# Optimization experiments

Hardware: AMD Instinct MI355X
Metric: run time of the kernel (lower is better)

The kernel has to match this reference:

```python
import jax, jax.numpy as jnp
import numpy as np

N_CHILDS = 50000
N_EDGES = 500000
NODE_FEAT = 256
NUM_SEM = 57
HID = 256
EDGE_FEAT = 64
EDGE_TYPES = 4
NUM_ITERS = 2


def setup_inputs() -> dict:
    key = jax.random.key(0)
    ks = jax.random.split(key, 12)
    d_in = NODE_FEAT + NUM_SEM            # 313
    d_ne = 2 * HID + EDGE_FEAT + EDGE_TYPES  # 580
    d_par = HID * (NUM_ITERS + 1)         # 768
    def lin(k, fan_in, fan_out):
        kw, kb = jax.random.split(k)
        s = 1.0 / np.sqrt(fan_in)
        return (jax.random.uniform(kw, (fan_in, fan_out), jnp.float32, -s, s),
                jax.random.uniform(kb, (fan_out,), jnp.float32, -s, s))
    W_child, b_child = lin(ks[0], d_in, HID)
    W_ne0, b_ne0 = lin(ks[1], d_ne, HID)
    W_ne1, b_ne1 = lin(ks[2], d_ne, HID)
    W_parent, b_parent = lin(ks[3], d_par, NODE_FEAT)
    return {
        "child_feats": jax.random.normal(ks[4], (1, N_CHILDS, d_in), jnp.float32),
        "child_exists": jnp.ones((1, N_CHILDS, 1), jnp.float32),
        "edge_type_onehot": jax.random.normal(ks[5], (1, N_EDGES, EDGE_TYPES), jnp.float32),
        "edge_feats": jax.random.normal(ks[6], (1, N_EDGES, EDGE_FEAT), jnp.float32),
        "edge_indices": jax.random.randint(ks[7], (1, N_EDGES, 2), 0, N_CHILDS, jnp.int64),
        "W_child": W_child, "b_child": b_child,
        "W_ne0": W_ne0, "b_ne0": b_ne0,
        "W_ne1": W_ne1, "b_ne1": b_ne1,
        "W_parent": W_parent, "b_parent": b_parent,
    }


def reference(child_feats, child_exists, edge_type_onehot, edge_feats, edge_indices,
              W_child, b_child, W_ne0, b_ne0, W_ne1, b_ne1, W_parent, b_parent):
    n = child_feats.shape[1]
    # node embedding: linear + relu, mask non-existent children
    x = jax.nn.relu(jnp.einsum('bnd,dh->bnh', child_feats, W_child) + b_child)
    x = x * child_exists                              # [1, N, H]
    iter_parent = [x.max(axis=1)]                     # symmetric_type == 'max'
    ef = jnp.concatenate([edge_type_onehot, edge_feats], axis=2)[0]  # [E, 4+64]
    src = edge_indices[0, :, 0]
    dst = edge_indices[0, :, 1]
    cnt = jax.ops.segment_sum(jnp.ones((src.shape[0],), x.dtype), src, num_segments=n)
    denom = jnp.maximum(cnt, 1.0)[:, None]            # scatter_mean clamp
    for W, b in ((W_ne0, b_ne0), (W_ne1, b_ne1)):
        nef = jnp.concatenate([x[0, src], x[0, dst], ef], axis=1)  # [E, 580]
        nef = jax.nn.relu(nef @ W + b)                # [E, H]
        # edge_symmetric_type == 'avg': scatter_mean over source index
        x = (jax.ops.segment_sum(nef, src, num_segments=n) / denom)[None]
        iter_parent.append(x.max(axis=1))
    parent = jnp.concatenate(iter_parent, axis=1)     # [1, H*(iters+1)]
    return jax.nn.relu(parent @ W_parent + b_parent)  # [1, node_feat_size]
```

## Files before the change

### kernel.cpp

```cpp
#include <hip/hip_runtime.h>

#define NC   50000
#define NE   500000
#define NEP  (NE + 64)
#define DIN  313
#define DNE  580
#define KPC  320
#define KB   96
#define NB_SCAN 196

typedef __attribute__((ext_vector_type(8))) short bf16x8;
typedef __attribute__((ext_vector_type(4))) float f32x4;

static __device__ __forceinline__ unsigned short f2bf(float f) {
    unsigned u = __float_as_uint(f);
    unsigned r = (u + 0x7fff + ((u >> 16) & 1)) >> 16;
    return (unsigned short)r;
}
static __device__ __forceinline__ float bf2f(unsigned short u) {
    return __uint_as_float(((unsigned)u) << 16);
}
static __device__ __forceinline__ void gload_lds16(const unsigned short* g, unsigned short* l) {
    __builtin_amdgcn_global_load_lds(
        (const __attribute__((address_space(1))) unsigned int*)(g),
        (__attribute__((address_space(3))) unsigned int*)(l), 16, 0, 0);
}

__global__ __launch_bounds__(256) void prep_w_kernel(
    const float* __restrict__ W0, const float* __restrict__ W1,
    const float* __restrict__ Wc,
    unsigned short* __restrict__ Wpt, unsigned short* __restrict__ Wbt,
    unsigned short* __restrict__ Wct)
{
    int b = blockIdx.x;
    if (b < 1024) {
        int layer = b >> 9, n2 = b & 511;
        const float* W = layer ? W1 : W0;
        unsigned short* dst = Wpt + (size_t)layer * 512 * 256 + (size_t)n2 * 256;
        int t = threadIdx.x;
        int ch = t >> 5, s = (t >> 3) & 3, j = t & 7;
        int gk = ch * 32 + ((s ^ (n2 & 3)) * 8) + j;
        float v = (n2 < 256) ? W[(size_t)gk * 256 + n2] : W[(size_t)(256 + gk) * 256 + (n2 - 256)];
        dst[t] = f2bf(v);
    } else if (b < 1536) {
        int idx = b - 1024;
        int layer = idx >> 8, n = idx & 255;
        const float* W = layer ? W1 : W0;
        unsigned short* dst = Wbt + (size_t)layer * 256 * KB + (size_t)n * KB;
        int t = threadIdx.x;
        if (t < KB) {
            int ch = t >> 5, s = (t >> 3) & 3, j = t & 7;
            int gk = ch * 32 + ((s ^ (n & 3)) * 8) + j;
            float v = (512 + gk < DNE) ? W[(size_t)(512 + gk) * 256 + n] : 0.0f;
            dst[t] = f2bf(v);
        }
    } else {
        int n = b - 1536;
        unsigned short* dst = Wct + (size_t)n * KPC;
        for (int t = threadIdx.x; t < KPC; t += 256) {
            int ch = t >> 5, s = (t >> 3) & 3, j = t & 7;
            int gk = ch * 32 + ((s ^ (n & 3)) * 8) + j;
            float v = (gk < DIN) ? Wc[(size_t)gk * 256 + n] : 0.0f;
            dst[t] = f2bf(v);
        }
    }
}

__global__ __launch_bounds__(256, 4) void child_mfma_kernel(
    const float* __restrict__ cf, const float* __restrict__ exists,
    const unsigned short* __restrict__ Wct, const float* __restrict__ bias,
    unsigned short* __restrict__ xb, float* __restrict__ pmax)
{
    __shared__ unsigned short sA[64][40];
    __shared__ unsigned short sB[256][32];
    __shared__ float smax[256];

    const int tid = threadIdx.x, lane = tid & 63, wid = tid >> 6;
    const int wm = wid >> 1, wn = wid & 1, l15 = lane & 15, l4 = lane >> 4;
    const int node0 = blockIdx.x * 64;
    const int arow = tid >> 2, s3 = tid & 3;

    smax[tid] = 0.0f;

    f32x4 acc[2][8];
    #pragma unroll
    for (int mi = 0; mi < 2; ++mi)
        #pragma unroll
        for (int ni = 0; ni < 8; ++ni)
            acc[mi][ni] = (f32x4){0.f, 0.f, 0.f, 0.f};

    int nodeA = node0 + arow; if (nodeA >= NC) nodeA = NC - 1;

    for (int ch = 0; ch < 10; ++ch) {
        #pragma unroll
        for (int i = 0; i < 4; ++i) {
            int n = (wid << 6) + (i << 4) + (lane >> 2);
            gload_lds16(Wct + (size_t)n * KPC + ch * 32 + (lane & 3) * 8,
                        &sB[(wid << 6) + (i << 4)][0]);
        }
        {
            int gk0 = ch * 32 + s3 * 8;
            union { unsigned short u[8]; int4 v; } pk;
            #pragma unroll
            for (int j = 0; j < 8; ++j) {
                int gk = gk0 + j;
                float f = (gk < DIN) ? cf[(size_t)nodeA * DIN + gk] : 0.0f;
                pk.u[j] = f2bf(f);
            }
            *(int4*)&sA[arow][s3 * 8] = pk.v;
        }
        __syncthreads();
        bf16x8 af[2];
        #pragma unroll
        for (int mi = 0; mi < 2; ++mi)
            af[mi] = *(const bf16x8*)&sA[wm * 32 + mi * 16 + l15][l4 * 8];
        #pragma unroll
        for (int ni = 0; ni < 8; ++ni) {
            int n = wn * 128 + ni * 16 + l15;
            bf16x8 bfr = *(const bf16x8*)&sB[n][(l4 ^ (n & 3)) * 8];
            acc[0][ni] = __builtin_amdgcn_mfma_f32_16x16x32_bf16(af[0], bfr, acc[0][ni], 0, 0, 0);
            acc[1][ni] = __builtin_amdgcn_mfma_f32_16x16x32_bf16(af[1], bfr, acc[1][ni], 0, 0, 0);
        }
        __syncthreads();
    }

    float bv[8];
    #pragma unroll
    for (int ni = 0; ni < 8; ++ni) bv[ni] = bias[wn * 128 + ni * 16 + l15];
    float cmax[8];
    #pragma unroll
    for (int ni = 0; ni < 8; ++ni) cmax[ni] = 0.0f;

    #pragma unroll
    for (int mi = 0; mi < 2; ++mi) {
        #pragma unroll
        for (int r = 0; r < 4; ++r) {
            int node = node0 + wm * 32 + mi * 16 + l4 * 4 + r;
            if (node < NC) {
                float ex = exists[node];
                #pragma unroll
                for (int ni = 0; ni < 8; ++ni) {
                    float v = fmaxf(acc[mi][ni][r] + bv[ni], 0.f) * ex;
                    xb[(size_t)node * 256 + wn * 128 + ni * 16 + l15] = f2bf(v);
                    cmax[ni] = fmaxf(cmax[ni], v);
                }
            }
        }
    }
    #pragma unroll
    for (int ni = 0; ni < 8; ++ni)
        atomicMax((unsigned int*)&smax[wn * 128 + ni * 16 + l15], __float_as_uint(cmax[ni]));
    __syncthreads();
    atomicMax((unsigned int*)&pmax[tid], __float_as_uint(smax[tid]));
}

__global__ __launch_bounds__(256, 3) void node_gemm_kernel(
    const unsigned short* __restrict__ xb,
    const unsigned short* __restrict__ Wpt,
    unsigned short* __restrict__ yp)
{
    __shared__ unsigned short sA[2][64][40];
    __shared__ unsigned short sB[2][256][32];

    const int tid = threadIdx.x, lane = tid & 63, wid = tid >> 6;
    const int wm = wid >> 1, wn = wid & 1, l15 = lane & 15, l4 = lane >> 4;
    const int node0 = blockIdx.x * 64;
    const int n0 = blockIdx.y * 256;
    const int arow = tid >> 2, s3 = tid & 3;

    int nodeA = node0 + arow; if (nodeA >= NC) nodeA = NC - 1;

    f32x4 acc[2][8];
    #pragma unroll
    for (int mi = 0; mi < 2; ++mi)
        #pragma unroll
        for (int ni = 0; ni < 8; ++ni)
            acc[mi][ni] = (f32x4){0.f, 0.f, 0.f, 0.f};

    #pragma unroll
    for (int i = 0; i < 4; ++i) {
        int n = (wid << 6) + (i << 4) + (lane >> 2);
        gload_lds16(Wpt + (size_t)(n0 + n) * 256 + (lane & 3) * 8, &sB[0][(wid << 6) + (i << 4)][0]);
    }
    *(int4*)&sA[0][arow][s3 * 8] = *(const int4*)(xb + (size_t)nodeA * 256 + s3 * 8);
    __syncthreads();

    int buf = 0;
    for (int ch = 0; ch < 8; ++ch) {
        const int nch = ch + 1;
        int4 areg;
        if (nch < 8) {
            #pragma unroll
            for (int i = 0; i < 4; ++i) {
                int n = (wid << 6) + (i << 4) + (lane >> 2);
                gload_lds16(Wpt + (size_t)(n0 + n) * 256 + nch * 32 + (lane & 3) * 8,
                            &sB[buf ^ 1][(wid << 6) + (i << 4)][0]);
            }
            areg = *(const int4*)(xb + (size_t)nodeA * 256 + nch * 32 + s3 * 8);
        }
        bf16x8 af[2];
        #pragma unroll
        for (int mi = 0; mi < 2; ++mi)
            af[mi] = *(const bf16x8*)&sA[buf][wm * 32 + mi * 16 + l15][l4 * 8];
        #pragma unroll
        for (int ni = 0; ni < 8; ++ni) {
            int n = wn * 128 + ni * 16 + l15;
            bf16x8 bfr = *(const bf16x8*)&sB[buf][n][(l4 ^ (n & 3)) * 8];
            acc[0][ni] = __builtin_amdgcn_mfma_f32_16x16x32_bf16(af[0], bfr, acc[0][ni], 0, 0, 0);
            acc[1][ni] = __builtin_amdgcn_mfma_f32_16x16x32_bf16(af[1], bfr, acc[1][ni], 0, 0, 0);
        }
        if (nch < 8) *(int4*)&sA[buf ^ 1][arow][s3 * 8] = areg;
        __syncthreads();
        buf ^= 1;
    }

    #pragma unroll
    for (int mi = 0; mi < 2; ++mi) {
        #pragma unroll
        for (int r = 0; r < 4; ++r) {
            int node = node0 + wm * 32 + mi * 16 + l4 * 4 + r;
            if (node < NC) {
                #pragma unroll
                for (int ni = 0; ni < 8; ++ni)
                    yp[(size_t)node * 512 + n0 + wn * 128 + ni * 16 + l15] = f2bf(acc[mi][ni][r]);
            }
        }
    }
}

__global__ __launch_bounds__(256) void count_int_kernel(
    const int* __restrict__ eidx, int* __restrict__ icnt)
{
    int t = blockIdx.x * 256 + threadIdx.x;
    if (t < NE) atomicAdd(&icnt[eidx[2 * t]], 1);
}

__global__ __launch_bounds__(256) void scan1_kernel(
    const int* __restrict__ icnt, int* __restrict__ part)
{
    __shared__ int sd[256];
    int i = blockIdx.x * 256 + threadIdx.x;
    sd[threadIdx.x] = (i < NC) ? icnt[i] : 0;
    __syncthreads();
    for (int d = 128; d > 0; d >>= 1) {
        if (threadIdx.x < d) sd[threadIdx.x] += sd[threadIdx.x + d];
        __syncthreads();
    }
    if (threadIdx.x == 0) part[blockIdx.x] = sd[0];
}

__global__ void scan2_kernel(int* __restrict__ part)
{
    if (threadIdx.x == 0) {
        int acc = 0;
        for (int i = 0; i < NB_SCAN; ++i) { int v = part[i]; part[i] = acc; acc += v; }
    }
}

__global__ __launch_bounds__(256) void scan3_kernel(
    const int* __restrict__ icnt, const int* __restrict__ part,
    int* __restrict__ cur)
{
    __shared__ int sc[256];
    const int t = threadIdx.x;
    int i = blockIdx.x * 256 + t;
    int val = (i < NC) ? icnt[i] : 0;
    sc[t] = val;
    __syncthreads();
    for (int d = 1; d < 256; d <<= 1) {
        int x = (t >= d) ? sc[t - d] : 0;
        __syncthreads();
        sc[t] += x;
        __syncthreads();
    }
    if (i < NC) cur[i] = part[blockIdx.x] + sc[t] - val;
}

__global__ __launch_bounds__(256) void bin_kernel(
    const int* __restrict__ eidx, int* __restrict__ cur, int* __restrict__ perm)
{
    int t = blockIdx.x * 256 + threadIdx.x;
    if (t < NE) {
        int s = eidx[2 * t];
        int p = atomicAdd(&cur[s], 1);
        perm[p] = t;
    }
}

__global__ __launch_bounds__(256) void inv_kernel(
    const int* __restrict__ icnt, float* __restrict__ inv)
{
    int t = blockIdx.x * 256 + threadIdx.x;
    if (t < NC) inv[t] = 1.0f / fmaxf((float)icnt[t], 1.0f);
}

__global__ __launch_bounds__(256) void ef_prep_kernel(
    const float* __restrict__ eto, const float* __restrict__ efe,
    const int* __restrict__ perm, const int* __restrict__ eidx,
    unsigned short* __restrict__ efc01, unsigned short* __restrict__ efc2,
    int* __restrict__ esrc, int* __restrict__ edst)
{
    int p = blockIdx.x * 256 + threadIdx.x;
    if (p >= NE) return;
    int e = perm[p];
    esrc[p] = eidx[2 * e];
    edst[p] = eidx[2 * e + 1];
    const float* efr = efe + (size_t)e * 64;

    union { unsigned short u[8]; int4 v; } pk;
    {
        float4 a = *(const float4*)(eto + (size_t)e * 4);
        float4 b = *(const float4*)(efr + 0);
        pk.u[0]=f2bf(a.x); pk.u[1]=f2bf(a.y); pk.u[2]=f2bf(a.z); pk.u[3]=f2bf(a.w);
        pk.u[4]=f2bf(b.x); pk.u[5]=f2bf(b.y); pk.u[6]=f2bf(b.z); pk.u[7]=f2bf(b.w);
        *(int4*)(efc01 + (size_t)p * 32) = pk.v;
    }
    #pragma unroll
    for (int g = 1; g < 4; ++g) {
        float4 a = *(const float4*)(efr + g * 8 - 4);
        float4 b = *(const float4*)(efr + g * 8);
        pk.u[0]=f2bf(a.x); pk.u[1]=f2bf(a.y); pk.u[2]=f2bf(a.z); pk.u[3]=f2bf(a.w);
        pk.u[4]=f2bf(b.x); pk.u[5]=f2bf(b.y); pk.u[6]=f2bf(b.z); pk.u[7]=f2bf(b.w);
        *(int4*)(efc01 + (size_t)p * 32 + g * 8) = pk.v;
    }
    #pragma unroll
    for (int g = 0; g < 4; ++g) {
        float4 a = *(const float4*)(efr + 28 + g * 8);
        float4 b = *(const float4*)(efr + 32 + g * 8);
        pk.u[0]=f2bf(a.x); pk.u[1]=f2bf(a.y); pk.u[2]=f2bf(a.z); pk.u[3]=f2bf(a.w);
        pk.u[4]=f2bf(b.x); pk.u[5]=f2bf(b.y); pk.u[6]=f2bf(b.z); pk.u[7]=f2bf(b.w);
        *(int4*)(efc01 + ((size_t)NEP + p) * 32 + g * 8) = pk.v;
    }
    {
        float4 a = *(const float4*)(efr + 60);
        pk.u[0]=f2bf(a.x); pk.u[1]=f2bf(a.y); pk.u[2]=f2bf(a.z); pk.u[3]=f2bf(a.w);
        pk.u[4]=0; pk.u[5]=0; pk.u[6]=0; pk.u[7]=0;
        *(int4*)(efc2 + (size_t)p * 8) = pk.v;
    }
}

#define LOAD16(B, YT, YM)                                              \
    _Pragma("unroll")                                                  \
    for (int r = 0; r < 16; ++r) {                                     \
        int row = (B) * 16 + r;                                        \
        YT[r] = bf2f(yp[((unsigned)s_src[row] << 9) + (unsigned)col]); \
        YM[r] = bf2f(yp[((unsigned)s_dst[row] << 9) + 256u + (unsigned)col]); \
    }

#define WALK16(B, YT, YM)                                              \
    _Pragma("unroll")                                                  \
    for (int r = 0; r < 16; ++r) {                                     \
        int row = (B) * 16 + r;                                        \
        float v = 0.0f;                                                \
        if (e0 + row < NE)                                             \
            v = fmaxf(bf2f(epb[row][col]) + YT[r] + YM[r] + b_col, 0.f); \
        int sr = s_src[row];                                           \
        if (sr != curn) {                                              \
            if (rstart > 0) accb[(size_t)curn * 256 + col] = run;      \
            else            atomicAdd(&accb[(size_t)curn * 256 + col], run); \
            curn = sr; run = v; rstart = row;                          \
        } else {                                                       \
            run += v;                                                  \
        }                                                              \
    }

__global__ __launch_bounds__(256, 4) void combine_efc_kernel(
    const unsigned short* __restrict__ yp,
    const unsigned short* __restrict__ efc01,
    const unsigned short* __restrict__ efc2,
    const int* __restrict__ esrc, const int* __restrict__ edst,
    const unsigned short* __restrict__ Wbt,
    const float* __restrict__ bias,
    float* __restrict__ accb)
{
    __shared__ __align__(16) unsigned char smem[34816];
    unsigned short (*sA01)[64][32] = (unsigned short (*)[64][32])(smem);
    unsigned short (*sA2)[8]       = (unsigned short (*)[8])(smem + 8192);
    unsigned short (*sW)[32]       = (unsigned short (*)[32])(smem + 9216);
    unsigned short (*epb)[272]     = (unsigned short (*)[272])(smem);
    __shared__ int s_src[64], s_dst[64];

    const int tid = threadIdx.x;
    const int nwg = gridDim.x;
    const int q = nwg >> 3, rr = nwg & 7;
    const int xcd = blockIdx.x & 7, within = blockIdx.x >> 3;
    const int bid = (xcd < rr ? xcd * (q + 1) : rr * (q + 1) + (xcd - rr) * q) + within;
    const int e0 = bid * 64;

    const int lane = tid & 63;
    const int wid  = tid >> 6;
    const int wm   = wid >> 1;
    const int wn   = wid & 1;
    const int l15  = lane & 15;
    const int l4   = lane >> 4;

    if (tid < 64) {
        int e = e0 + tid; if (e > NE - 1) e = NE - 1;
        s_src[tid] = esrc[e];
        s_dst[tid] = edst[e];
    }
    gload_lds16(efc01 + ((size_t)e0 + wid * 16) * 32 + lane * 8, &sA01[0][wid * 16][0]);
    gload_lds16(efc01 + ((size_t)NEP + e0 + wid * 16) * 32 + lane * 8, &sA01[1][wid * 16][0]);
    if (wid == 0)
        gload_lds16(efc2 + (size_t)e0 * 8 + lane * 8, &sA2[0][0]);
    #pragma unroll
    for (int i = 0; i < 4; ++i) {
        gload_lds16(Wbt + (size_t)((wid << 6) + (i << 4) + (lane >> 2)) * KB + (lane & 3) * 8,
                    &sW[(wid << 6) + (i << 4)][0]);
    }
    __syncthreads();

    f32x4 acc[2][8];
    #pragma unroll
    for (int mi = 0; mi < 2; ++mi)
        #pragma unroll
        for (int ni = 0; ni < 8; ++ni)
            acc[mi][ni] = (f32x4){0.f, 0.f, 0.f, 0.f};

    #pragma unroll
    for (int ch = 0; ch < 3; ++ch) {
        if (ch > 0) {
            __syncthreads();
            #pragma unroll
            for (int i = 0; i < 4; ++i) {
                gload_lds16(Wbt + (size_t)((wid << 6) + (i << 4) + (lane >> 2)) * KB + ch * 32 + (lane & 3) * 8,
                            &sW[(wid << 6) + (i << 4)][0]);
            }
            __syncthreads();
        }
        bf16x8 af0, af1;
        if (ch < 2) {
            af0 = *(const bf16x8*)&sA01[ch][wm * 32 + l15][l4 * 8];
            af1 = *(const bf16x8*)&sA01[ch][wm * 32 + 16 + l15][l4 * 8];
        } else {
            bf16x8 z = (bf16x8){0,0,0,0,0,0,0,0};
            bf16x8 a0 = *(const bf16x8*)&sA2[wm * 32 + l15][0];
            bf16x8 a1 = *(const bf16x8*)&sA2[wm * 32 + 16 + l15][0];
            af0 = (l4 == 0) ? a0 : z;
            af1 = (l4 == 0) ? a1 : z;
        }
        #pragma unroll
        for (int ni = 0; ni < 8; ++ni) {
            int n = wn * 128 + ni * 16 + l15;
            bf16x8 bfr = *(const bf16x8*)&sW[n][(l4 ^ (n & 3)) * 8];
            acc[0][ni] = __builtin_amdgcn_mfma_f32_16x16x32_bf16(af0, bfr, acc[0][ni], 0, 0, 0);
            acc[1][ni] = __builtin_amdgcn_mfma_f32_16x16x32_bf16(af1, bfr, acc[1][ni], 0, 0, 0);
        }
    }
    __syncthreads();

    #pragma unroll
    for (int mi = 0; mi < 2; ++mi)
        #pragma unroll
        for (int ni = 0; ni < 8; ++ni)
            #pragma unroll
            for (int r = 0; r < 4; ++r)
                epb[wm * 32 + mi * 16 + l4 * 4 + r][wn * 128 + ni * 16 + l15] = f2bf(acc[mi][ni][r]);

    const int col = tid;
    const float b_col = bias[col];
    float ytA[16], ymA[16], ytB[16], ymB[16];
    LOAD16(0, ytA, ymA)
    LOAD16(1, ytB, ymB)
    __syncthreads();

    int curn = s_src[0];
    int rstart = 0;
    float run = 0.f;

    WALK16(0, ytA, ymA)
    LOAD16(2, ytA, ymA)
    WALK16(1, ytB, ymB)
    LOAD16(3, ytB, ymB)
    WALK16(2, ytA, ymA)
    WALK16(3, ytB, ymB)

    atomicAdd(&accb[(size_t)curn * 256 + col], run);
}

__global__ __launch_bounds__(256, 3) void combine_f32_kernel(
    const unsigned short* __restrict__ yp,
    const float* __restrict__ eto, const float* __restrict__ efe,
    const int* __restrict__ eidx, const int* __restrict__ perm,
    const unsigned short* __restrict__ Wbt,
    const float* __restrict__ bias,
    float* __restrict__ accb)
{
    __shared__ unsigned short sA[3][64][40];
    __shared__ unsigned short sW[2][256][32];
    __shared__ int s_src[64], s_dst[64], s_perm[64];

    const int tid = threadIdx.x;
    const int nwg = gridDim.x;
    const int q = nwg >> 3, rr = nwg & 7;
    const int xcd = blockIdx.x & 7, within = blockIdx.x >> 3;
    const int bid = (xcd < rr ? xcd * (q + 1) : rr * (q + 1) + (xcd - rr) * q) + within;
    const int e0 = bid * 64;

    if (tid < 64) {
        int ee = e0 + tid; if (ee >= NE) ee = NE - 1;
        int e = perm[ee];
        s_perm[tid] = e;
        s_src[tid] = eidx[2 * e];
        s_dst[tid] = eidx[2 * e + 1];
    }
    const int lane = tid & 63;
    const int wid  = tid >> 6;
    const int wm   = wid >> 1;
    const int wn   = wid & 1;
    const int l15  = lane & 15;
    const int l4   = lane >> 4;
    const int arow = tid >> 2;
    const int s3   = tid & 3;

    f32x4 acc[2][8];
    #pragma unroll
    for (int mi = 0; mi < 2; ++mi)
        #pragma unroll
        for (int ni = 0; ni < 8; ++ni)
            acc[mi][ni] = (f32x4){0.f, 0.f, 0.f, 0.f};

    #pragma unroll
    for (int i = 0; i < 4; ++i) {
        int n = (wid << 6) + (i << 4) + (lane >> 2);
        gload_lds16(Wbt + (size_t)n * KB + (lane & 3) * 8, &sW[0][(wid << 6) + (i << 4)][0]);
    }
    __syncthreads();

    const int my_e = s_perm[arow];
    #pragma unroll
    for (int ch = 0; ch < 3; ++ch) {
        int g0 = ch * 32 + s3 * 8;
        union { unsigned short u[8]; int4 v; } pk;
        #pragma unroll
        for (int j = 0; j < 8; ++j) {
            int g = g0 + j;
            float f = 0.0f;
            if (g < 4)       f = eto[(size_t)my_e * 4 + g];
            else if (g < 68) f = efe[(size_t)my_e * 64 + (g - 4)];
            pk.u[j] = f2bf(f);
        }
        *(int4*)&sA[ch][arow][s3 * 8] = pk.v;
    }
    __syncthreads();

    int buf = 0;
    #pragma unroll
    for (int ch = 0; ch < 3; ++ch) {
        if (ch + 1 < 3) {
            #pragma unroll
            for (int i = 0; i < 4; ++i) {
                int n = (wid << 6) + (i << 4) + (lane >> 2);
                gload_lds16(Wbt + (size_t)n * KB + (ch + 1) * 32 + (lane & 3) * 8,
                            &sW[buf ^ 1][(wid << 6) + (i << 4)][0]);
            }
        }
        bf16x8 af[2];
        #pragma unroll
        for (int mi = 0; mi < 2; ++mi)
            af[mi] = *(const bf16x8*)&sA[ch][wm * 32 + mi * 16 + l15][l4 * 8];
        #pragma unroll
        for (int ni = 0; ni < 8; ++ni) {
            int n = wn * 128 + ni * 16 + l15;
            bf16x8 bfr = *(const bf16x8*)&sW[buf][n][(l4 ^ (n & 3)) * 8];
            acc[0][ni] = __builtin_amdgcn_mfma_f32_16x16x32_bf16(af[0], bfr, acc[0][ni], 0, 0, 0);
            acc[1][ni] = __builtin_amdgcn_mfma_f32_16x16x32_bf16(af[1], bfr, acc[1][ni], 0, 0, 0);
        }
        __syncthreads();
        buf ^= 1;
    }

    float (*ep)[258] = (float (*)[258])(&sW[0][0][0]);
    const int col = tid;
    const float b_col = bias[col];

    int curn = s_src[0];
    int rstart = 0;
    float run = 0.f;
    #pragma unroll
    for (int c = 0; c < 4; ++c) {
        if (wm == (c >> 1)) {
            const int mi = c & 1;
            #pragma unroll
            for (int ni = 0; ni < 8; ++ni) {
                #pragma unroll
                for (int r = 0; r < 4; ++r)
                    ep[l4 * 4 + r][wn * 128 + ni * 16 + l15] = acc[mi][ni][r];
            }
        }
        float yt[16], ym[16];
        #pragma unroll
        for (int r = 0; r < 16; ++r) {
            int row = c * 16 + r;
            yt[r] = bf2f(yp[(size_t)s_src[row] * 512 + col]);
            ym[r] = bf2f(yp[(size_t)s_dst[row] * 512 + 256 + col]);
        }
        __syncthreads();
        #pragma unroll
        for (int r = 0; r < 16; ++r) {
            int row = c * 16 + r;
            float v = 0.0f;
            if (e0 + row < NE)
                v = fmaxf(ep[r][col] + yt[r] + ym[r] + b_col, 0.f);
            int sr = s_src[row];
            if (sr != curn) {
                if (rstart > 0) accb[(size_t)curn * 256 + col] = run;
                else            atomicAdd(&accb[(size_t)curn * 256 + col], run);
                curn = sr; run = v; rstart = row;
            } else {
                run += v;
            }
        }
        __syncthreads();
    }
    atomicAdd(&accb[(size_t)curn * 256 + col], run);
}

__global__ __launch_bounds__(256) void finalize_kernel(
    const float* __restrict__ src, const float* __restrict__ inv,
    unsigned short* __restrict__ xb_out, float* __restrict__ pmax, int n)
{
    const int tid = threadIdx.x;
    int i0 = blockIdx.x * 128;
    int iend = i0 + 128; if (iend > n) iend = n;
    float m = 0.0f;
    for (int i = i0; i < iend; ++i) {
        float v = src[(size_t)i * 256 + tid];
        v *= inv[i];
        xb_out[(size_t)i * 256 + tid] = f2bf(v);
        m = fmaxf(m, v);
    }
    atomicMax((unsigned int*)&pmax[tid], __float_as_uint(m));
}

__global__ __launch_bounds__(256) void parent_kernel(
    const float* __restrict__ pmax, const float* __restrict__ W,
    const float* __restrict__ bias, float* __restrict__ out)
{
    __shared__ float sp[768];
    const int tid = threadIdx.x;
    for (int i = tid; i < 768; i += 256) sp[i] = pmax[i];
    __syncthreads();
    float s = bias[tid];
    for (int k = 0; k < 768; ++k) s = fmaf(sp[k], W[(size_t)k * 256 + tid], s);
    out[tid] = fmaxf(s, 0.f);
}

extern "C" void kernel_launch(void* const* d_in, const int* in_sizes, int n_in,
                              void* d_out, int out_size, void* d_ws, size_t ws_size,
                              hipStream_t stream)
{
    const float* cf   = (const float*)d_in[0];
    const float* ex   = (const float*)d_in[1];
    const float* eto  = (const float*)d_in[2];
    const float* efe  = (const float*)d_in[3];
    const int*   eidx = (const int*)d_in[4];
    const float* Wc   = (const float*)d_in[5];
    const float* bc   = (const float*)d_in[6];
    const float* W0   = (const float*)d_in[7];
    const float* b0   = (const float*)d_in[8];
    const float* W1   = (const float*)d_in[9];
    const float* b1   = (const float*)d_in[10];
    const float* Wp   = (const float*)d_in[11];
    const float* bp   = (const float*)d_in[12];

    float*          accb = (float*)d_ws;
    float*          invv = accb + (size_t)NC * 256;
    float*          pmax = invv + NC;
    unsigned short* xb   = (unsigned short*)(pmax + 768);
    unsigned short* yp   = xb + (size_t)NC * 256;
    unsigned short* Wpt  = yp + (size_t)NC * 512;
    unsigned short* Wbt  = Wpt + (size_t)2 * 512 * 256;
    unsigned short* Wct  = Wbt + (size_t)2 * 256 * KB;
    int*            icnt = (int*)(Wct + (size_t)256 * KPC);
    int*            part = icnt + NC;
    int*            curb = part + 256;
    int*            perm = curb + NC;
    unsigned short* efc01 = (unsigned short*)(perm + NE);
    unsigned short* efc2  = efc01 + (size_t)2 * NEP * 32;
    int*            esrc  = (int*)(efc2 + (size_t)NEP * 8);
    int*            edst  = esrc + NE;
    size_t need = (size_t)((char*)(edst + NE) - (char*)d_ws);
    const bool use_efc = (ws_size >= need);

    hipMemsetAsync(pmax, 0, 768 * sizeof(float), stream);
    hipMemsetAsync(icnt, 0, NC * sizeof(int), stream);

    prep_w_kernel<<<1792, 256, 0, stream>>>(W0, W1, Wc, Wpt, Wbt, Wct);
    child_mfma_kernel<<<(NC + 63) / 64, 256, 0, stream>>>(cf, ex, Wct, bc, xb, pmax);

    count_int_kernel<<<(NE + 255) / 256, 256, 0, stream>>>(eidx, icnt);
    scan1_kernel<<<NB_SCAN, 256, 0, stream>>>(icnt, part);
    scan2_kernel<<<1, 64, 0, stream>>>(part);
    scan3_kernel<<<NB_SCAN, 256, 0, stream>>>(icnt, part, curb);
    bin_kernel<<<(NE + 255) / 256, 256, 0, stream>>>(eidx, curb, perm);
    inv_kernel<<<(NC + 255) / 256, 256, 0, stream>>>(icnt, invv);
    if (use_efc)
        ef_prep_kernel<<<(NE + 255) / 256, 256, 0, stream>>>(eto, efe, perm, eidx, efc01, efc2, esrc, edst);

    const int nwg = (NE + 63) / 64;
    for (int it = 0; it < 2; ++it) {
        node_gemm_kernel<<<dim3((NC + 63) / 64, 2), 256, 0, stream>>>(
            xb, Wpt + (size_t)it * 512 * 256, yp);
        hipMemsetAsync(accb, 0, (size_t)NC * 256 * sizeof(float), stream);
        if (use_efc)
            combine_efc_kernel<<<nwg, 256, 0, stream>>>(
                yp, efc01, efc2, esrc, edst,
                Wbt + (size_t)it * 256 * KB, it ? b1 : b0, accb);
        else
            combine_f32_kernel<<<nwg, 256, 0, stream>>>(
                yp, eto, efe, eidx, perm,
                Wbt + (size_t)it * 256 * KB, it ? b1 : b0, accb);
        finalize_kernel<<<(NC + 127) / 128, 256, 0, stream>>>(accb, invv, xb, pmax + 256 * (it + 1), NC);
    }
    parent_kernel<<<1, 256, 0, stream>>>(pmax, Wp, bp, (float*)d_out);
}
```

Measured before the change: 624.7 us.

## Fuse mean-scaling into second node GEMM and cache repeated source loads

Adds a node GEMM that reads the fp32 scatter accumulator, scales each row by its inverse count and converts to bf16 while staging A tiles, so the separate finalize pass no longer has to write bf16 node features. The finalize step becomes a max-only reduction. The combine kernel also skips reloading the source-node projection when consecutive sorted edges share a source. Trade-off: the GEMM now reads fp32 instead of bf16 input, and the max pass still reads the whole accumulator.

```diff
diff --git a/kernel.cpp b/kernel.cpp
--- a/kernel.cpp
+++ b/kernel.cpp
@@ -228,6 +228,94 @@
     }
 }
 
+__global__ __launch_bounds__(256, 3) void node_gemm_scaled_kernel(
+    const float* __restrict__ accb, const float* __restrict__ invv,
+    const unsigned short* __restrict__ Wpt,
+    unsigned short* __restrict__ yp)
+{
+    __shared__ unsigned short sA[2][64][40];
+    __shared__ unsigned short sB[2][256][32];
+
+    const int tid = threadIdx.x, lane = tid & 63, wid = tid >> 6;
+    const int wm = wid >> 1, wn = wid & 1, l15 = lane & 15, l4 = lane >> 4;
+    const int node0 = blockIdx.x * 64;
+    const int n0 = blockIdx.y * 256;
+    const int arow = tid >> 2, s3 = tid & 3;
+
+    int nodeA = node0 + arow; if (nodeA >= NC) nodeA = NC - 1;
+    const float inv_n = invv[nodeA];
+
+    f32x4 acc[2][8];
+    #pragma unroll
+    for (int mi = 0; mi < 2; ++mi)
+        #pragma unroll
+        for (int ni = 0; ni < 8; ++ni)
+            acc[mi][ni] = (f32x4){0.f, 0.f, 0.f, 0.f};
+
+    #pragma unroll
+    for (int i = 0; i < 4; ++i) {
+        int n = (wid << 6) + (i << 4) + (lane >> 2);
+        gload_lds16(Wpt + (size_t)(n0 + n) * 256 + (lane & 3) * 8, &sB[0][(wid << 6) + (i << 4)][0]);
+    }
+    {
+        float4 a0 = *(const float4*)(accb + (size_t)nodeA * 256 + s3 * 8);
+        float4 a1 = *(const float4*)(accb + (size_t)nodeA * 256 + s3 * 8 + 4);
+        union { unsigned short u[8]; int4 v; } pk;
+        pk.u[0]=f2bf(a0.x*inv_n); pk.u[1]=f2bf(a0.y*inv_n); pk.u[2]=f2bf(a0.z*inv_n); pk.u[3]=f2bf(a0.w*inv_n);
+        pk.u[4]=f2bf(a1.x*inv_n); pk.u[5]=f2bf(a1.y*inv_n); pk.u[6]=f2bf(a1.z*inv_n); pk.u[7]=f2bf(a1.w*inv_n);
+        *(int4*)&sA[0][arow][s3 * 8] = pk.v;
+    }
+    __syncthreads();
+
+    int buf = 0;
+    for (int ch = 0; ch < 8; ++ch) {
+        const int nch = ch + 1;
+        float4 f4a, f4b;
+        if (nch < 8) {
+            #pragma unroll
+            for (int i = 0; i < 4; ++i) {
+                int n = (wid << 6) + (i << 4) + (lane >> 2);
+                gload_lds16(Wpt + (size_t)(n0 + n) * 256 + nch * 32 + (lane & 3) * 8,
+                            &sB[buf ^ 1][(wid << 6) + (i << 4)][0]);
+            }
+            f4a = *(const float4*)(accb + (size_t)nodeA * 256 + nch * 32 + s3 * 8);
+            f4b = *(const float4*)(accb + (size_t)nodeA * 256 + nch * 32 + s3 * 8 + 4);
+        }
+        bf16x8 af[2];
+        #pragma unroll
+        for (int mi = 0; mi < 2; ++mi)
+            af[mi] = *(const bf16x8*)&sA[buf][wm * 32 + mi * 16 + l15][l4 * 8];
+        #pragma unroll
+        for (int ni = 0; ni < 8; ++ni) {
+            int n = wn * 128 + ni * 16 + l15;
+            bf16x8 bfr = *(const bf16x8*)&sB[buf][n][(l4 ^ (n & 3)) * 8];
+            acc[0][ni] = __builtin_amdgcn_mfma_f32_16x16x32_bf16(af[0], bfr, acc[0][ni], 0, 0, 0);
+            acc[1][ni] = __builtin_amdgcn_mfma_f32_16x16x32_bf16(af[1], bfr, acc[1][ni], 0, 0, 0);
+        }
+        if (nch < 8) {
+            union { unsigned short u[8]; int4 v; } pk;
+            pk.u[0]=f2bf(f4a.x*inv_n); pk.u[1]=f2bf(f4a.y*inv_n); pk.u[2]=f2bf(f4a.z*inv_n); pk.u[3]=f2bf(f4a.w*inv_n);
+            pk.u[4]=f2bf(f4b.x*inv_n); pk.u[5]=f2bf(f4b.y*inv_n); pk.u[6]=f2bf(f4b.z*inv_n); pk.u[7]=f2bf(f4b.w*inv_n);
+            *(int4*)&sA[buf ^ 1][arow][s3 * 8] = pk.v;
+        }
+        __syncthreads();
+        buf ^= 1;
+    }
+
+    #pragma unroll
+    for (int mi = 0; mi < 2; ++mi) {
+        #pragma unroll
+        for (int r = 0; r < 4; ++r) {
+            int node = node0 + wm * 32 + mi * 16 + l4 * 4 + r;
+            if (node < NC) {
+                #pragma unroll
+                for (int ni = 0; ni < 8; ++ni)
+                    yp[(size_t)node * 512 + n0 + wn * 128 + ni * 16 + l15] = f2bf(acc[mi][ni][r]);
+            }
+        }
+    }
+}
+
 __global__ __launch_bounds__(256) void count_int_kernel(
     const int* __restrict__ eidx, int* __restrict__ icnt)
 {
@@ -343,7 +431,12 @@
     _Pragma("unroll")                                                  \
     for (int r = 0; r < 16; ++r) {                                     \
         int row = (B) * 16 + r;                                        \
-        YT[r] = bf2f(yp[((unsigned)s_src[row] << 9) + (unsigned)col]); \
+        int sr_ = s_src[row];                                          \
+        if (sr_ != ldsrc) {                   \
+            ytPrev = bf2f(yp[((unsigned)sr_ << 9) + (unsigned)col]);   \
+            ldsrc = sr_;                                               \
+        }                                                              \
+        YT[r] = ytPrev;                                                \
         YM[r] = bf2f(yp[((unsigned)s_dst[row] << 9) + 256u + (unsigned)col]); \
     }
 
@@ -459,6 +552,8 @@
 
     const int col = tid;
     const float b_col = bias[col];
+    int ldsrc = -1;
+    float ytPrev = 0.f;
     float ytA[16], ymA[16], ytB[16], ymB[16];
     LOAD16(0, ytA, ymA)
     LOAD16(1, ytB, ymB)
@@ -630,6 +725,19 @@
         xb_out[(size_t)i * 256 + tid] = f2bf(v);
         m = fmaxf(m, v);
     }
+    atomicMax((unsigned int*)&pmax[tid], __float_as_uint(m));
+}
+
+__global__ __launch_bounds__(256) void pmax_only_kernel(
+    const float* __restrict__ src, const float* __restrict__ inv,
+    float* __restrict__ pmax, int n)
+{
+    const int tid = threadIdx.x;
+    int i0 = blockIdx.x * 128;
+    int iend = i0 + 128; if (iend > n) iend = n;
+    float m = 0.0f;
+    for (int i = i0; i < iend; ++i)
+        m = fmaxf(m, src[(size_t)i * 256 + tid] * inv[i]);
     atomicMax((unsigned int*)&pmax[tid], __float_as_uint(m));
 }
 
@@ -699,19 +807,28 @@
         ef_prep_kernel<<<(NE + 255) / 256, 256, 0, stream>>>(eto, efe, perm, eidx, efc01, efc2, esrc, edst);
 
     const int nwg = (NE + 63) / 64;
-    for (int it = 0; it < 2; ++it) {
-        node_gemm_kernel<<<dim3((NC + 63) / 64, 2), 256, 0, stream>>>(
-            xb, Wpt + (size_t)it * 512 * 256, yp);
+    if (use_efc) {
+        node_gemm_kernel<<<dim3((NC + 63) / 64, 2), 256, 0, stream>>>(xb, Wpt, yp);
         hipMemsetAsync(accb, 0, (size_t)NC * 256 * sizeof(float), stream);
-        if (use_efc)
-            combine_efc_kernel<<<nwg, 256, 0, stream>>>(
-                yp, efc01, efc2, esrc, edst,
-                Wbt + (size_t)it * 256 * KB, it ? b1 : b0, accb);
-        else
+        combine_efc_kernel<<<nwg, 256, 0, stream>>>(
+            yp, efc01, efc2, esrc, edst, Wbt, b0, accb);
+        pmax_only_kernel<<<(NC + 127) / 128, 256, 0, stream>>>(accb, invv, pmax + 256, NC);
+        node_gemm_scaled_kernel<<<dim3((NC + 63) / 64, 2), 256, 0, stream>>>(
+            accb, invv, Wpt + (size_t)512 * 256, yp);
+        hipMemsetAsync(accb, 0, (size_t)NC * 256 * sizeof(float), stream);
+        combine_efc_kernel<<<nwg, 256, 0, stream>>>(
+            yp, efc01, efc2, esrc, edst, Wbt + (size_t)256 * KB, b1, accb);
+        pmax_only_kernel<<<(NC + 127) / 128, 256, 0, stream>>>(accb, invv, pmax + 512, NC);
+    } else {
+        for (int it = 0; it < 2; ++it) {
+            node_gemm_kernel<<<dim3((NC + 63) / 64, 2), 256, 0, stream>>>(
+                xb, Wpt + (size_t)it * 512 * 256, yp);
+            hipMemsetAsync(accb, 0, (size_t)NC * 256 * sizeof(float), stream);
             combine_f32_kernel<<<nwg, 256, 0, stream>>>(
                 yp, eto, efe, eidx, perm,
                 Wbt + (size_t)it * 256 * KB, it ? b1 : b0, accb);
-        finalize_kernel<<<(NC + 127) / 128, 256, 0, stream>>>(accb, invv, xb, pmax + 256 * (it + 1), NC);
+            finalize_kernel<<<(NC + 127) / 128, 256, 0, stream>>>(accb, invv, xb, pmax + 256 * (it + 1), NC);
+        }
     }
     parent_kernel<<<1, 256, 0, stream>>>(pmax, Wp, bp, (float*)d_out);
 }
```

New measurement: 658.2 us. 5.3% more time.
